# Optimization experiments

Hardware: AMD Instinct MI355X
Metric: run time of the kernel (lower is better)

## Reference

```python
import jax, jax.numpy as jnp
import numpy as np

B, S_F, S_H, S_W = 1, 4, 32, 32
S = S_F * S_H * S_W            # 4096 video tokens
DIM, HEADS = 1536, 12
HD = DIM // HEADS              # 128
EPS = 1e-6


def _rope_angles(max_pos, dim_half):
    inv = 1.0 / (10000.0 ** (np.arange(dim_half, dtype=np.float32) / dim_half))
    return (np.arange(max_pos, dtype=np.float32)[:, None] * inv[None, :]).astype(np.float32)


def setup_inputs():
    key = jax.random.key(0)
    ks = jax.random.split(key, 6)
    w = lambda k: jax.random.normal(k, (DIM, DIM), jnp.float32) * (DIM ** -0.5)
    c = HD // 2
    f0, f1 = c - 2 * (c // 3), c // 3   # 22, 21 (Wan rope split for F/H/W)
    freqs = jnp.asarray(np.concatenate(
        [_rope_angles(1024, f0), _rope_angles(1024, f1), _rope_angles(1024, f1)], axis=1))
    return dict(
        x=jax.random.normal(ks[0], (B, S, DIM), jnp.float32),
        seq_lens=jnp.full((B,), S, jnp.int32),
        grid_sizes=jnp.array([[S_F, S_H, S_W]], jnp.int32),
        freqs=freqs,
        t=500,
        Wq=w(ks[1]), bq=jnp.zeros((DIM,), jnp.float32),
        Wk=w(ks[2]), bk=jnp.zeros((DIM,), jnp.float32),
        Wv=w(ks[3]), bv=jnp.zeros((DIM,), jnp.float32),
        Wo=w(ks[4]), bo=jnp.zeros((DIM,), jnp.float32),
        gq=jnp.ones((DIM,), jnp.float32),
        gk=jnp.ones((DIM,), jnp.float32),
    )


def _rmsnorm(x, g):
    return x * jax.lax.rsqrt(jnp.mean(x * x, axis=-1, keepdims=True) + EPS) * g


def _rope_apply(x, cos, sin):
    # x: [B,S,n,d]; cos/sin: [S, d//2]; rotate interleaved (even, odd) pairs
    b, s, n, d = x.shape
    xr = x.reshape(b, s, n, d // 2, 2)
    xe, xo = xr[..., 0], xr[..., 1]
    c = cos[None, :, None, :]
    sn = sin[None, :, None, :]
    return jnp.stack([xe * c - xo * sn, xe * sn + xo * c], axis=-1).reshape(b, s, n, d)


def _rope_tables(grid_sizes, freqs):
    F, H, W = [int(v) for v in np.asarray(grid_sizes)[0]]
    c = HD // 2
    f0, f1 = c - 2 * (c // 3), c // 3
    ang = jnp.concatenate([
        jnp.broadcast_to(freqs[:F, :f0][:, None, None, :], (F, H, W, f0)),
        jnp.broadcast_to(freqs[:H, f0:f0 + f1][None, :, None, :], (F, H, W, f1)),
        jnp.broadcast_to(freqs[:W, f0 + f1:][None, None, :, :], (F, H, W, f1)),
    ], axis=-1).reshape(F * H * W, c)  # [S, d//2]
    return jnp.cos(ang), jnp.sin(ang)


def reference(x, seq_lens, grid_sizes, freqs, t, Wq, bq, Wk, bk, Wv, bv, Wo, bo, gq, gk):
    b, s = x.shape[:2]
    cos, sin = _rope_tables(grid_sizes, freqs)

    q = _rmsnorm(x @ Wq.T + bq, gq).reshape(b, s, HEADS, HD)
    k = _rmsnorm(x @ Wk.T + bk, gk).reshape(b, s, HEADS, HD)
    v = (x @ Wv.T + bv).reshape(b, s, HEADS, HD)
    q = _rope_apply(q, cos, sin)
    k = _rope_apply(k, cos, sin)

    scores = jnp.einsum('bqhd,bkhd->bhqk', q, k) * (HD ** -0.5)  # [B,H,S,S]
    kmask = jnp.arange(s)[None, :] < seq_lens[:, None]           # varlen key mask
    scores = jnp.where(kmask[:, None, None, :], scores, -jnp.inf)
    attn = jax.nn.softmax(scores, axis=-1)
    out = jnp.einsum('bhqk,bkhd->bqhd', attn, v).reshape(b, s, DIM)
    return out @ Wo.T + bo
```

## Files before the change

### kernel.cpp

```cpp
#include <hip/hip_runtime.h>
#include <hip/hip_bf16.h>

#define S 4096
#define DIM 1536
#define HEADS 12
#define HD 128
#define CHALF 64
#define NQKV 4608

typedef unsigned short u16;
typedef unsigned int u32;
typedef __attribute__((ext_vector_type(8))) short bf16x8;
typedef __attribute__((ext_vector_type(4))) float f32x4;
typedef __attribute__((ext_vector_type(16))) float f32x16;

__device__ __forceinline__ u16 f2b(float f) {
    u32 u = __float_as_uint(f);
    u32 r = (u + 0x7fffu + ((u >> 16) & 1u)) >> 16;
    return (u16)r;
}
__device__ __forceinline__ float b2f(u16 b) {
    return __uint_as_float(((u32)b) << 16);
}
__device__ __forceinline__ u32 pack2(float a, float b) {
    u32 lo = (__float_as_uint(a) + 0x8000u) >> 16;
    u32 hi = (__float_as_uint(b) + 0x8000u) & 0xffff0000u;
    return lo | hi;
}
__device__ __forceinline__ void gld_lds16(const u16* g, u16* l) {
    __builtin_amdgcn_global_load_lds((const __attribute__((address_space(1))) void*)g,
                                     (__attribute__((address_space(3))) void*)l, 16, 0, 0);
}

__global__ void k_cvt_all(const float4* __restrict__ x, const float4* __restrict__ wq,
                          const float4* __restrict__ wk, const float4* __restrict__ wv,
                          const float4* __restrict__ wo,
                          ushort4* __restrict__ xb, ushort4* __restrict__ wqkv,
                          ushort4* __restrict__ wob) {
    const int N4X = S * DIM / 4, N4W = DIM * DIM / 4;
    int i = blockIdx.x * 256 + threadIdx.x;
    const float4* src; ushort4* dst; int off;
    if (i < N4X) { src = x; dst = xb; off = i; }
    else {
        int j = i - N4X;
        int w = j / N4W; off = j - w * N4W;
        if (w == 0)      { src = wq; dst = wqkv; }
        else if (w == 1) { src = wk; dst = wqkv + N4W; }
        else if (w == 2) { src = wv; dst = wqkv + 2 * N4W; }
        else             { src = wo; dst = wob; }
    }
    float4 v = src[off];
    ushort4 o;
    o.x = f2b(v.x); o.y = f2b(v.y); o.z = f2b(v.z); o.w = f2b(v.w);
    dst[off] = o;
}

__global__ void k_tables(const float* __restrict__ freqs, const int* __restrict__ grid_sizes,
                         float* __restrict__ cosT, float* __restrict__ sinT) {
    int idx = blockIdx.x * 256 + threadIdx.x;
    if (idx >= S * CHALF) return;
    int s = idx >> 6;
    int i = idx & 63;
    int H = grid_sizes[1], W = grid_sizes[2];
    int hw = H * W;
    int f = s / hw;
    int rem = s - f * hw;
    int h = rem / W;
    int w = rem - h * W;
    const int f0 = 22, f1 = 21;
    int pos = (i < f0) ? f : ((i < f0 + f1) ? h : w);
    float ang = freqs[pos * CHALF + i];
    cosT[idx] = cosf(ang);
    sinT[idx] = sinf(ang);
}

template<int OUT_BF16, int QKV>
__global__ __launch_bounds__(256, 2) void k_gemm(const u16* __restrict__ A, const u16* __restrict__ W,
                                                 const float* __restrict__ b0, const float* __restrict__ b1,
                                                 const float* __restrict__ b2,
                                                 void* __restrict__ Cout, int N, int K, int ldc) {
    __shared__ u16 As[128 * 32];
    __shared__ u16 Bs[128 * 32];
    int tid = threadIdx.x;
    int lane = tid & 63, wave = tid >> 6;
    int wm = wave >> 1, wn = wave & 1;
    int quad = lane >> 4, l16 = lane & 15;
    int rowBase = blockIdx.y * 128;
    int colBase = blockIdx.x * 128;
    int lr = lane >> 2, lc = (lane & 3) << 3;

    f32x4 acc[4][4] = {};

    for (int kb = 0; kb < K; kb += 32) {
        __syncthreads();
#pragma unroll
        for (int c = 0; c < 2; c++) {
            int rrel = wave * 32 + c * 16;
            gld_lds16(A + (size_t)(rowBase + rrel + lr) * K + kb + lc, As + rrel * 32);
            gld_lds16(W + (size_t)(colBase + rrel + lr) * K + kb + lc, Bs + rrel * 32);
        }
        __syncthreads();

        bf16x8 a[4], b[4];
#pragma unroll
        for (int mi = 0; mi < 4; mi++)
            a[mi] = *(const bf16x8*)(As + (wm * 64 + mi * 16 + l16) * 32 + quad * 8);
#pragma unroll
        for (int ni = 0; ni < 4; ni++)
            b[ni] = *(const bf16x8*)(Bs + (wn * 64 + ni * 16 + l16) * 32 + quad * 8);
#pragma unroll
        for (int mi = 0; mi < 4; mi++)
#pragma unroll
            for (int ni = 0; ni < 4; ni++)
                acc[mi][ni] = __builtin_amdgcn_mfma_f32_16x16x32_bf16(a[mi], b[ni], acc[mi][ni], 0, 0, 0);
    }

#pragma unroll
    for (int mi = 0; mi < 4; mi++) {
#pragma unroll
        for (int ni = 0; ni < 4; ni++) {
            int col = colBase + wn * 64 + ni * 16 + l16;
            float bv;
            if (QKV) {
                int third = colBase / DIM;
                const float* bp = (third == 0) ? b0 : ((third == 1) ? b1 : b2);
                bv = bp[col - third * DIM];
            } else {
                bv = b0[col];
            }
#pragma unroll
            for (int r = 0; r < 4; r++) {
                int row = rowBase + wm * 64 + mi * 16 + quad * 4 + r;
                float v = acc[mi][ni][r] + bv;
                if (OUT_BF16)
                    ((u16*)Cout)[(size_t)row * ldc + col] = f2b(v);
                else
                    ((float*)Cout)[(size_t)row * ldc + col] = v;
            }
        }
    }
}

__global__ __launch_bounds__(256) void k_normrope(u16* __restrict__ qkvp, const float* __restrict__ gq,
                                                  const float* __restrict__ gk,
                                                  const float* __restrict__ cosT, const float* __restrict__ sinT,
                                                  float qscale) {
    int s = blockIdx.x;
    int which = blockIdx.y;
    const float* g = which ? gk : gq;
    float scale = which ? 1.0f : qscale;
    int tid = threadIdx.x;
    int lane = tid & 63, wave = tid >> 6;
    u32* row = (u32*)(qkvp + (size_t)s * NQKV + which * DIM);

    int w0 = tid, w1 = tid + 256, w2 = tid + 512;
    u32 p0 = row[w0], p1 = row[w1], p2 = row[w2];
    float e0 = b2f(p0 & 0xffff), o0 = b2f(p0 >> 16);
    float e1 = b2f(p1 & 0xffff), o1 = b2f(p1 >> 16);
    float e2 = b2f(p2 & 0xffff), o2 = b2f(p2 >> 16);
    float ss = e0 * e0 + o0 * o0 + e1 * e1 + o1 * o1 + e2 * e2 + o2 * o2;

    __shared__ float wsum[4];
    for (int off = 32; off; off >>= 1) ss += __shfl_down(ss, off);
    if (lane == 0) wsum[wave] = ss;
    __syncthreads();
    float tot = wsum[0] + wsum[1] + wsum[2] + wsum[3];
    float r = rsqrtf(tot * (1.0f / DIM) + 1e-6f) * scale;

    const float* cr = cosT + (size_t)s * CHALF;
    const float* sr = sinT + (size_t)s * CHALF;
#pragma unroll
    for (int j = 0; j < 3; j++) {
        int p = (j == 0) ? w0 : (j == 1) ? w1 : w2;
        float e = (j == 0) ? e0 : (j == 1) ? e1 : e2;
        float o = (j == 0) ? o0 : (j == 1) ? o1 : o2;
        int i = p & 63;
        float c = cr[i], sn = sr[i];
        e = e * r * g[2 * p];
        o = o * r * g[2 * p + 1];
        float ne = e * c - o * sn;
        float no = e * sn + o * c;
        row[p] = (u32)f2b(ne) | ((u32)f2b(no) << 16);
    }
}

__global__ void k_transpose(const u16* __restrict__ src, u16* __restrict__ dst) {
    __shared__ u16 t[32][33];
    int bx = blockIdx.x;
    int by = blockIdx.y;
    int tx = threadIdx.x, ty = threadIdx.y;
#pragma unroll
    for (int i = 0; i < 4; i++)
        t[ty + i * 8][tx] = src[(size_t)(by * 32 + ty + i * 8) * NQKV + bx * 32 + tx];
    __syncthreads();
#pragma unroll
    for (int i = 0; i < 4; i++)
        dst[(size_t)(bx * 32 + ty + i * 8) * S + by * 32 + tx] = t[tx][ty + i * 8];
}

#define FM 16.5f
__global__ __launch_bounds__(256, 3) void k_attn(const u16* __restrict__ qkv, const u16* __restrict__ vt,
                                                 u16* __restrict__ O0, u16* __restrict__ O1,
                                                 float* __restrict__ lT,
                                                 const int* __restrict__ seq_lens) {
    int h = blockIdx.y;
    int q0 = blockIdx.x * 128;
    int p = blockIdx.z;
    int kh0 = p * (S / 2);
    int tid = threadIdx.x;
    int lane = tid & 63, wave = tid >> 6;
    int l31 = lane & 31, hi = lane >> 5;
    int seqlen = seq_lens[0];
    u16* Op = p ? O1 : O0;

    __shared__ u16 Ks[64 * 136];
    __shared__ u16 Vs[128 * 88];

    int qrow = q0 + wave * 32 + l31;
    bf16x8 qf[8];
#pragma unroll
    for (int c = 0; c < 8; c++)
        qf[c] = *(const bf16x8*)(qkv + (size_t)qrow * NQKV + h * HD + c * 16 + hi * 8);

    f32x16 o_acc[4] = {};
    float lsum = 0.f;

    for (int kt = 0; kt < S / 2; kt += 64) {
        int kbase = kh0 + kt;
        __syncthreads();
        {
            int r = tid >> 2, cc = (tid & 3) * 32;
            const u16* gk_ = qkv + (size_t)(kbase + r) * NQKV + DIM + h * HD + cc;
            u16* dk = Ks + r * 136 + cc;
#pragma unroll
            for (int u = 0; u < 4; u++)
                *(uint4*)(dk + u * 8) = *(const uint4*)(gk_ + u * 8);
            int dr = tid >> 3, dc = (tid & 7) * 8;
#pragma unroll
            for (int it = 0; it < 4; it++)
                *(uint4*)(Vs + (dr + it * 32) * 88 + dc) =
                    *(const uint4*)(vt + (size_t)(h * HD + dr + it * 32) * S + kbase + dc);
        }
        __syncthreads();

        f32x16 sc0 = {}, sc1 = {};
#pragma unroll
        for (int c = 0; c < 8; c++) {
            bf16x8 kf0 = *(const bf16x8*)(Ks + l31 * 136 + c * 16 + hi * 8);
            bf16x8 kf1 = *(const bf16x8*)(Ks + (32 + l31) * 136 + c * 16 + hi * 8);
            sc0 = __builtin_amdgcn_mfma_f32_32x32x16_bf16(kf0, qf[c], sc0, 0, 0, 0);
            sc1 = __builtin_amdgcn_mfma_f32_32x32x16_bf16(kf1, qf[c], sc1, 0, 0, 0);
        }

        bool tail = (kbase + 64 > seqlen);
        bf16x8 pfrag[4];
#pragma unroll
        for (int b = 0; b < 2; b++) {
            f32x16 s16 = b ? sc1 : sc0;
            u32 pk[4][2];
            if (!tail) {
#pragma unroll
                for (int g = 0; g < 4; g++) {
                    float e0 = __builtin_amdgcn_exp2f(s16[4 * g + 0] - FM);
                    float e1 = __builtin_amdgcn_exp2f(s16[4 * g + 1] - FM);
                    float e2 = __builtin_amdgcn_exp2f(s16[4 * g + 2] - FM);
                    float e3 = __builtin_amdgcn_exp2f(s16[4 * g + 3] - FM);
                    lsum += (e0 + e1) + (e2 + e3);
                    pk[g][0] = pack2(e0, e1);
                    pk[g][1] = pack2(e2, e3);
                }
            } else {
#pragma unroll
                for (int g = 0; g < 4; g++) {
                    float e[4];
#pragma unroll
                    for (int r = 0; r < 4; r++) {
                        int key = kbase + b * 32 + r + 8 * g + 4 * hi;
                        float v = __builtin_amdgcn_exp2f(s16[4 * g + r] - FM);
                        e[r] = (key < seqlen) ? v : 0.f;
                        lsum += e[r];
                    }
                    pk[g][0] = pack2(e[0], e[1]);
                    pk[g][1] = pack2(e[2], e[3]);
                }
            }
#pragma unroll
            for (int cc = 0; cc < 2; cc++) {
                int g0 = 2 * cc, g1 = 2 * cc + 1;
                u32 own0 = hi ? pk[g1][0] : pk[g0][0];
                u32 own1 = hi ? pk[g1][1] : pk[g0][1];
                u32 snd0 = hi ? pk[g0][0] : pk[g1][0];
                u32 snd1 = hi ? pk[g0][1] : pk[g1][1];
                u32 rcv0 = (u32)__shfl_xor((int)snd0, 32);
                u32 rcv1 = (u32)__shfl_xor((int)snd1, 32);
                union { u32 u[4]; bf16x8 v; } cvt2;
                cvt2.u[0] = hi ? rcv0 : own0;
                cvt2.u[1] = hi ? rcv1 : own1;
                cvt2.u[2] = hi ? own0 : rcv0;
                cvt2.u[3] = hi ? own1 : rcv1;
                pfrag[b * 2 + cc] = cvt2.v;
            }
        }

#pragma unroll
        for (int db = 0; db < 4; db++) {
#pragma unroll
            for (int c4 = 0; c4 < 4; c4++) {
                bf16x8 vf = *(const bf16x8*)(Vs + (db * 32 + l31) * 88 + c4 * 16 + hi * 8);
                o_acc[db] = __builtin_amdgcn_mfma_f32_32x32x16_bf16(vf, pfrag[c4], o_acc[db], 0, 0, 0);
            }
        }
    }

    float l_all = lsum + __shfl_xor(lsum, 32);
    float linv = 1.0f / l_all;
#pragma unroll
    for (int db = 0; db < 4; db++) {
#pragma unroll
        for (int g = 0; g < 4; g++) {
            int d0 = db * 32 + 8 * g + 4 * hi;
            u16 o4[4];
#pragma unroll
            for (int r = 0; r < 4; r++)
                o4[r] = f2b(o_acc[db][4 * g + r] * linv);
            *(uint2*)(Op + (size_t)qrow * DIM + h * HD + d0) = *(const uint2*)o4;
        }
    }
    if (!hi) lT[((size_t)p * HEADS + h) * S + qrow] = l_all;
}

__global__ __launch_bounds__(384) void k_combine(u16* __restrict__ O0, const u16* __restrict__ O1,
                                                 const float* __restrict__ lT) {
    int q = blockIdx.x;
    int tid = threadIdx.x;
    int h = tid >> 5;
    size_t base = (size_t)q * DIM + tid * 4;
    float l0 = lT[(size_t)h * S + q];
    float l1 = lT[(size_t)(HEADS + h) * S + q];
    float inv = 1.0f / (l0 + l1);
    float c0 = l0 * inv, c1 = l1 * inv;
    uint2 u0 = *(const uint2*)(O0 + base);
    uint2 u1 = *(const uint2*)(O1 + base);
    const u16* a = (const u16*)&u0;
    const u16* b = (const u16*)&u1;
    u16 o[4];
#pragma unroll
    for (int i = 0; i < 4; i++)
        o[i] = f2b(c0 * b2f(a[i]) + c1 * b2f(b[i]));
    *(uint2*)(O0 + base) = *(uint2*)o;
}

extern "C" void kernel_launch(void* const* d_in, const int* in_sizes, int n_in,
                              void* d_out, int out_size, void* d_ws, size_t ws_size,
                              hipStream_t stream) {
    const float* x = (const float*)d_in[0];
    const int* seq_lens = (const int*)d_in[1];
    const int* grid_sizes = (const int*)d_in[2];
    const float* freqs = (const float*)d_in[3];
    const float* Wq = (const float*)d_in[5];
    const float* bq = (const float*)d_in[6];
    const float* Wk = (const float*)d_in[7];
    const float* bk = (const float*)d_in[8];
    const float* Wv = (const float*)d_in[9];
    const float* bv = (const float*)d_in[10];
    const float* Wo = (const float*)d_in[11];
    const float* bo = (const float*)d_in[12];
    const float* gq = (const float*)d_in[13];
    const float* gk = (const float*)d_in[14];
    float* out = (float*)d_out;

    char* w = (char*)d_ws;
    u16* xb    = (u16*)w; w += (size_t)S * DIM * 2;
    u16* qkv   = (u16*)w; w += (size_t)S * NQKV * 2;
    u16* Wqkvb = (u16*)w; w += (size_t)3 * DIM * DIM * 2;
    u16* Wob   = (u16*)w; w += (size_t)DIM * DIM * 2;
    u16* ab    = (u16*)w; w += (size_t)S * DIM * 2;
    u16* O1    = (u16*)w; w += (size_t)S * DIM * 2;
    float* cosT = (float*)w; w += (size_t)S * CHALF * 4;
    float* sinT = (float*)w; w += (size_t)S * CHALF * 4;
    float* lT  = (float*)w; w += (size_t)2 * HEADS * S * 4;
    u16* vt = Wqkvb;

    const float qscale = 0.08838834764831845f * 1.44269504088896341f;

    const int N4X = S * DIM / 4, N4W = DIM * DIM / 4;
    k_cvt_all<<<(N4X + 4 * N4W) / 256, 256, 0, stream>>>(
        (const float4*)x, (const float4*)Wq, (const float4*)Wk, (const float4*)Wv, (const float4*)Wo,
        (ushort4*)xb, (ushort4*)Wqkvb, (ushort4*)Wob);
    k_tables<<<(S * CHALF + 255) / 256, 256, 0, stream>>>(freqs, grid_sizes, cosT, sinT);

    k_gemm<1, 1><<<dim3(NQKV / 128, S / 128), 256, 0, stream>>>(
        xb, Wqkvb, bq, bk, bv, qkv, NQKV, DIM, NQKV);

    k_normrope<<<dim3(S, 2), 256, 0, stream>>>(qkv, gq, gk, cosT, sinT, qscale);

    k_transpose<<<dim3(DIM / 32, S / 32), dim3(32, 8), 0, stream>>>(qkv + 2 * DIM, vt);

    k_attn<<<dim3(S / 128, HEADS, 2), 256, 0, stream>>>(qkv, vt, ab, O1, lT, seq_lens);

    k_combine<<<S, 384, 0, stream>>>(ab, O1, lT);

    k_gemm<0, 0><<<dim3(DIM / 128, S / 128), 256, 0, stream>>>(
        ab, Wob, bo, bo, bo, out, DIM, DIM, DIM);
}
```

Before: 429.9 us.

## Split attention keys four ways, swizzle LDS with direct loads, narrow output GEMM tile

The attention kernel now splits the key range into four parts instead of two, which doubles the block count and raises the occupancy hint to 4. The partial outputs are written into buffers that are no longer needed (xb and the V slot of qkv), and the combine step is extended to merge all four. K and V tiles are now loaded straight into LDS with an XOR swizzle instead of padded rows. The output projection uses a 128x64 tile so more blocks are launched. The costs are extra combine traffic and more partial-result writes.

```diff
diff --git a/kernel.cpp b/kernel.cpp
--- a/kernel.cpp
+++ b/kernel.cpp
@@ -74,52 +74,65 @@
     sinT[idx] = sinf(ang);
 }
 
-template<int OUT_BF16, int QKV>
+template<int TN, int OUT_BF16, int QKV>
 __global__ __launch_bounds__(256, 2) void k_gemm(const u16* __restrict__ A, const u16* __restrict__ W,
                                                  const float* __restrict__ b0, const float* __restrict__ b1,
                                                  const float* __restrict__ b2,
                                                  void* __restrict__ Cout, int N, int K, int ldc) {
     __shared__ u16 As[128 * 32];
-    __shared__ u16 Bs[128 * 32];
+    __shared__ u16 Bs[TN * 32];
     int tid = threadIdx.x;
     int lane = tid & 63, wave = tid >> 6;
-    int wm = wave >> 1, wn = wave & 1;
     int quad = lane >> 4, l16 = lane & 15;
     int rowBase = blockIdx.y * 128;
-    int colBase = blockIdx.x * 128;
+    int colBase = blockIdx.x * TN;
     int lr = lane >> 2, lc = (lane & 3) << 3;
 
-    f32x4 acc[4][4] = {};
+    constexpr int MI = (TN == 128) ? 4 : 2;
+    int wm = (TN == 128) ? (wave >> 1) : wave;
+    int wn = (TN == 128) ? (wave & 1) : 0;
+
+    f32x4 acc[MI][4] = {};
 
     for (int kb = 0; kb < K; kb += 32) {
         __syncthreads();
-#pragma unroll
-        for (int c = 0; c < 2; c++) {
-            int rrel = wave * 32 + c * 16;
-            gld_lds16(A + (size_t)(rowBase + rrel + lr) * K + kb + lc, As + rrel * 32);
-            gld_lds16(W + (size_t)(colBase + rrel + lr) * K + kb + lc, Bs + rrel * 32);
+        if (TN == 128) {
+#pragma unroll
+            for (int c = 0; c < 2; c++) {
+                int rrel = wave * 32 + c * 16;
+                gld_lds16(A + (size_t)(rowBase + rrel + lr) * K + kb + lc, As + rrel * 32);
+                gld_lds16(W + (size_t)(colBase + rrel + lr) * K + kb + lc, Bs + rrel * 32);
+            }
+        } else {
+            gld_lds16(A + (size_t)(rowBase + wave * 32 + lr) * K + kb + lc, As + (wave * 32) * 32);
+            gld_lds16(A + (size_t)(rowBase + wave * 32 + 16 + lr) * K + kb + lc, As + (wave * 32 + 16) * 32);
+            gld_lds16(W + (size_t)(colBase + wave * 16 + lr) * K + kb + lc, Bs + (wave * 16) * 32);
         }
         __syncthreads();
 
-        bf16x8 a[4], b[4];
-#pragma unroll
-        for (int mi = 0; mi < 4; mi++)
-            a[mi] = *(const bf16x8*)(As + (wm * 64 + mi * 16 + l16) * 32 + quad * 8);
-#pragma unroll
-        for (int ni = 0; ni < 4; ni++)
-            b[ni] = *(const bf16x8*)(Bs + (wn * 64 + ni * 16 + l16) * 32 + quad * 8);
-#pragma unroll
-        for (int mi = 0; mi < 4; mi++)
+        bf16x8 a[MI], b[4];
+#pragma unroll
+        for (int mi = 0; mi < MI; mi++) {
+            int row = (TN == 128) ? (wm * 64 + mi * 16 + l16) : (wave * 32 + mi * 16 + l16);
+            a[mi] = *(const bf16x8*)(As + row * 32 + quad * 8);
+        }
+#pragma unroll
+        for (int ni = 0; ni < 4; ni++) {
+            int row = (TN == 128) ? (wn * 64 + ni * 16 + l16) : (ni * 16 + l16);
+            b[ni] = *(const bf16x8*)(Bs + row * 32 + quad * 8);
+        }
+#pragma unroll
+        for (int mi = 0; mi < MI; mi++)
 #pragma unroll
             for (int ni = 0; ni < 4; ni++)
                 acc[mi][ni] = __builtin_amdgcn_mfma_f32_16x16x32_bf16(a[mi], b[ni], acc[mi][ni], 0, 0, 0);
     }
 
 #pragma unroll
-    for (int mi = 0; mi < 4; mi++) {
+    for (int mi = 0; mi < MI; mi++) {
 #pragma unroll
         for (int ni = 0; ni < 4; ni++) {
-            int col = colBase + wn * 64 + ni * 16 + l16;
+            int col = colBase + ((TN == 128) ? wn * 64 : 0) + ni * 16 + l16;
             float bv;
             if (QKV) {
                 int third = colBase / DIM;
@@ -130,7 +143,7 @@
             }
 #pragma unroll
             for (int r = 0; r < 4; r++) {
-                int row = rowBase + wm * 64 + mi * 16 + quad * 4 + r;
+                int row = rowBase + ((TN == 128) ? wm * 64 : wave * 32) + mi * 16 + quad * 4 + r;
                 float v = acc[mi][ni][r] + bv;
                 if (OUT_BF16)
                     ((u16*)Cout)[(size_t)row * ldc + col] = f2b(v);
@@ -199,22 +212,32 @@
 }
 
 #define FM 16.5f
-__global__ __launch_bounds__(256, 3) void k_attn(const u16* __restrict__ qkv, const u16* __restrict__ vt,
+__global__ __launch_bounds__(256, 4) void k_attn(const u16* __restrict__ qkv, const u16* __restrict__ vt,
                                                  u16* __restrict__ O0, u16* __restrict__ O1,
+                                                 u16* __restrict__ O2, u16* __restrict__ O3,
                                                  float* __restrict__ lT,
                                                  const int* __restrict__ seq_lens) {
     int h = blockIdx.y;
     int q0 = blockIdx.x * 128;
     int p = blockIdx.z;
-    int kh0 = p * (S / 2);
+    int kh0 = p * (S / 4);
     int tid = threadIdx.x;
     int lane = tid & 63, wave = tid >> 6;
     int l31 = lane & 31, hi = lane >> 5;
+    int l31x = l31 & 7;
     int seqlen = seq_lens[0];
-    u16* Op = p ? O1 : O0;
-
-    __shared__ u16 Ks[64 * 136];
-    __shared__ u16 Vs[128 * 88];
+
+    __shared__ u16 Ks[64 * 128];
+    __shared__ u16 Vs[128 * 64];
+
+    size_t koff_[4], voff_[4];
+#pragma unroll
+    for (int it = 0; it < 4; it++) {
+        int kr = wave * 16 + it * 4 + (lane >> 4);
+        koff_[it] = (size_t)kr * NQKV + DIM + h * HD + (((lane & 15) ^ (kr & 7)) << 3);
+        int vr = wave * 32 + it * 8 + (lane >> 3);
+        voff_[it] = (size_t)(h * HD + vr) * S + (((lane & 7) ^ (vr & 7)) << 3);
+    }
 
     int qrow = q0 + wave * 32 + l31;
     bf16x8 qf[8];
@@ -225,29 +248,26 @@
     f32x16 o_acc[4] = {};
     float lsum = 0.f;
 
-    for (int kt = 0; kt < S / 2; kt += 64) {
+    for (int kt = 0; kt < S / 4; kt += 64) {
         int kbase = kh0 + kt;
         __syncthreads();
         {
-            int r = tid >> 2, cc = (tid & 3) * 32;
-            const u16* gk_ = qkv + (size_t)(kbase + r) * NQKV + DIM + h * HD + cc;
-            u16* dk = Ks + r * 136 + cc;
-#pragma unroll
-            for (int u = 0; u < 4; u++)
-                *(uint4*)(dk + u * 8) = *(const uint4*)(gk_ + u * 8);
-            int dr = tid >> 3, dc = (tid & 7) * 8;
+            size_t kb = (size_t)kbase * NQKV;
 #pragma unroll
             for (int it = 0; it < 4; it++)
-                *(uint4*)(Vs + (dr + it * 32) * 88 + dc) =
-                    *(const uint4*)(vt + (size_t)(h * HD + dr + it * 32) * S + kbase + dc);
+                gld_lds16(qkv + kb + koff_[it], Ks + (wave * 16 + it * 4) * 128);
+#pragma unroll
+            for (int it = 0; it < 4; it++)
+                gld_lds16(vt + kbase + voff_[it], Vs + (wave * 32 + it * 8) * 64);
         }
         __syncthreads();
 
         f32x16 sc0 = {}, sc1 = {};
 #pragma unroll
         for (int c = 0; c < 8; c++) {
-            bf16x8 kf0 = *(const bf16x8*)(Ks + l31 * 136 + c * 16 + hi * 8);
-            bf16x8 kf1 = *(const bf16x8*)(Ks + (32 + l31) * 136 + c * 16 + hi * 8);
+            int j = 2 * c + hi;
+            bf16x8 kf0 = *(const bf16x8*)(Ks + l31 * 128 + ((j ^ l31x) << 3));
+            bf16x8 kf1 = *(const bf16x8*)(Ks + (32 + l31) * 128 + ((j ^ l31x) << 3));
             sc0 = __builtin_amdgcn_mfma_f32_32x32x16_bf16(kf0, qf[c], sc0, 0, 0, 0);
             sc1 = __builtin_amdgcn_mfma_f32_32x32x16_bf16(kf1, qf[c], sc1, 0, 0, 0);
         }
@@ -306,11 +326,15 @@
         for (int db = 0; db < 4; db++) {
 #pragma unroll
             for (int c4 = 0; c4 < 4; c4++) {
-                bf16x8 vf = *(const bf16x8*)(Vs + (db * 32 + l31) * 88 + c4 * 16 + hi * 8);
+                int j = 2 * c4 + hi;
+                bf16x8 vf = *(const bf16x8*)(Vs + (db * 32 + l31) * 64 + ((j ^ l31x) << 3));
                 o_acc[db] = __builtin_amdgcn_mfma_f32_32x32x16_bf16(vf, pfrag[c4], o_acc[db], 0, 0, 0);
             }
         }
     }
+
+    u16* Op = (p == 0) ? O0 : (p == 1) ? O1 : (p == 2) ? O2 : O3;
+    size_t ldO = (p == 3) ? NQKV : DIM;
 
     float l_all = lsum + __shfl_xor(lsum, 32);
     float linv = 1.0f / l_all;
@@ -323,31 +347,39 @@
 #pragma unroll
             for (int r = 0; r < 4; r++)
                 o4[r] = f2b(o_acc[db][4 * g + r] * linv);
-            *(uint2*)(Op + (size_t)qrow * DIM + h * HD + d0) = *(const uint2*)o4;
+            *(uint2*)(Op + (size_t)qrow * ldO + h * HD + d0) = *(const uint2*)o4;
         }
     }
     if (!hi) lT[((size_t)p * HEADS + h) * S + qrow] = l_all;
 }
 
 __global__ __launch_bounds__(384) void k_combine(u16* __restrict__ O0, const u16* __restrict__ O1,
+                                                 const u16* __restrict__ O2, const u16* __restrict__ O3,
                                                  const float* __restrict__ lT) {
     int q = blockIdx.x;
     int tid = threadIdx.x;
     int h = tid >> 5;
-    size_t base = (size_t)q * DIM + tid * 4;
-    float l0 = lT[(size_t)h * S + q];
-    float l1 = lT[(size_t)(HEADS + h) * S + q];
-    float inv = 1.0f / (l0 + l1);
-    float c0 = l0 * inv, c1 = l1 * inv;
-    uint2 u0 = *(const uint2*)(O0 + base);
-    uint2 u1 = *(const uint2*)(O1 + base);
+    float l0 = lT[(size_t)(0 * HEADS + h) * S + q];
+    float l1 = lT[(size_t)(1 * HEADS + h) * S + q];
+    float l2 = lT[(size_t)(2 * HEADS + h) * S + q];
+    float l3 = lT[(size_t)(3 * HEADS + h) * S + q];
+    float inv = 1.0f / (l0 + l1 + l2 + l3);
+    float c0 = l0 * inv, c1 = l1 * inv, c2 = l2 * inv, c3 = l3 * inv;
+    size_t b0 = (size_t)q * DIM + tid * 4;
+    size_t b3 = (size_t)q * NQKV + tid * 4;
+    uint2 u0 = *(const uint2*)(O0 + b0);
+    uint2 u1 = *(const uint2*)(O1 + b0);
+    uint2 u2 = *(const uint2*)(O2 + b0);
+    uint2 u3 = *(const uint2*)(O3 + b3);
     const u16* a = (const u16*)&u0;
     const u16* b = (const u16*)&u1;
+    const u16* c = (const u16*)&u2;
+    const u16* d = (const u16*)&u3;
     u16 o[4];
 #pragma unroll
     for (int i = 0; i < 4; i++)
-        o[i] = f2b(c0 * b2f(a[i]) + c1 * b2f(b[i]));
-    *(uint2*)(O0 + base) = *(uint2*)o;
+        o[i] = f2b(c0 * b2f(a[i]) + c1 * b2f(b[i]) + c2 * b2f(c[i]) + c3 * b2f(d[i]));
+    *(uint2*)(O0 + b0) = *(uint2*)o;
 }
 
 extern "C" void kernel_launch(void* const* d_in, const int* in_sizes, int n_in,
@@ -378,8 +410,10 @@
     u16* O1    = (u16*)w; w += (size_t)S * DIM * 2;
     float* cosT = (float*)w; w += (size_t)S * CHALF * 4;
     float* sinT = (float*)w; w += (size_t)S * CHALF * 4;
-    float* lT  = (float*)w; w += (size_t)2 * HEADS * S * 4;
+    float* lT  = (float*)w; w += (size_t)4 * HEADS * S * 4;
     u16* vt = Wqkvb;
+    u16* O2 = xb;
+    u16* O3 = qkv + 2 * DIM;
 
     const float qscale = 0.08838834764831845f * 1.44269504088896341f;
 
@@ -389,17 +423,17 @@
         (ushort4*)xb, (ushort4*)Wqkvb, (ushort4*)Wob);
     k_tables<<<(S * CHALF + 255) / 256, 256, 0, stream>>>(freqs, grid_sizes, cosT, sinT);
 
-    k_gemm<1, 1><<<dim3(NQKV / 128, S / 128), 256, 0, stream>>>(
+    k_gemm<128, 1, 1><<<dim3(NQKV / 128, S / 128), 256, 0, stream>>>(
         xb, Wqkvb, bq, bk, bv, qkv, NQKV, DIM, NQKV);
 
     k_normrope<<<dim3(S, 2), 256, 0, stream>>>(qkv, gq, gk, cosT, sinT, qscale);
 
     k_transpose<<<dim3(DIM / 32, S / 32), dim3(32, 8), 0, stream>>>(qkv + 2 * DIM, vt);
 
-    k_attn<<<dim3(S / 128, HEADS, 2), 256, 0, stream>>>(qkv, vt, ab, O1, lT, seq_lens);
-
-    k_combine<<<S, 384, 0, stream>>>(ab, O1, lT);
-
-    k_gemm<0, 0><<<dim3(DIM / 128, S / 128), 256, 0, stream>>>(
+    k_attn<<<dim3(S / 128, HEADS, 4), 256, 0, stream>>>(qkv, vt, ab, O1, O2, O3, lT, seq_lens);
+
+    k_combine<<<S, 384, 0, stream>>>(ab, O1, O2, O3, lT);
+
+    k_gemm<64, 0, 0><<<dim3(DIM / 64, S / 128), 256, 0, stream>>>(
         ab, Wob, bo, bo, bo, out, DIM, DIM, DIM);
 }
```

New measurement: 713.9 us. 66.1% more time.

## Prefetch next K/V tile into registers in attention; narrow output GEMM tiles

Applied to the files above, without the earlier changes.

The attention kernel now loads the next K and V tile from global memory into registers while the current tile is being computed, and stores those registers to shared memory at the start of the next iteration. This hides global load latency behind MFMA work. Its occupancy hint rises from 3 to 4 blocks per CU. The output projection GEMM moves to a 128x64 tile variant, which doubles its grid to 384 blocks for better CU fill, at the cost of less reuse per block. The extra prefetch registers may cause spills or stop the higher occupancy target from being reached.

```diff
diff --git a/kernel.cpp b/kernel.cpp
--- a/kernel.cpp
+++ b/kernel.cpp
@@ -74,52 +74,65 @@
     sinT[idx] = sinf(ang);
 }
 
-template<int OUT_BF16, int QKV>
+template<int TN, int OUT_BF16, int QKV>
 __global__ __launch_bounds__(256, 2) void k_gemm(const u16* __restrict__ A, const u16* __restrict__ W,
                                                  const float* __restrict__ b0, const float* __restrict__ b1,
                                                  const float* __restrict__ b2,
                                                  void* __restrict__ Cout, int N, int K, int ldc) {
     __shared__ u16 As[128 * 32];
-    __shared__ u16 Bs[128 * 32];
+    __shared__ u16 Bs[TN * 32];
     int tid = threadIdx.x;
     int lane = tid & 63, wave = tid >> 6;
-    int wm = wave >> 1, wn = wave & 1;
     int quad = lane >> 4, l16 = lane & 15;
     int rowBase = blockIdx.y * 128;
-    int colBase = blockIdx.x * 128;
+    int colBase = blockIdx.x * TN;
     int lr = lane >> 2, lc = (lane & 3) << 3;
 
-    f32x4 acc[4][4] = {};
+    constexpr int MI = (TN == 128) ? 4 : 2;
+    int wm = (TN == 128) ? (wave >> 1) : wave;
+    int wn = (TN == 128) ? (wave & 1) : 0;
+
+    f32x4 acc[MI][4] = {};
 
     for (int kb = 0; kb < K; kb += 32) {
         __syncthreads();
-#pragma unroll
-        for (int c = 0; c < 2; c++) {
-            int rrel = wave * 32 + c * 16;
-            gld_lds16(A + (size_t)(rowBase + rrel + lr) * K + kb + lc, As + rrel * 32);
-            gld_lds16(W + (size_t)(colBase + rrel + lr) * K + kb + lc, Bs + rrel * 32);
+        if (TN == 128) {
+#pragma unroll
+            for (int c = 0; c < 2; c++) {
+                int rrel = wave * 32 + c * 16;
+                gld_lds16(A + (size_t)(rowBase + rrel + lr) * K + kb + lc, As + rrel * 32);
+                gld_lds16(W + (size_t)(colBase + rrel + lr) * K + kb + lc, Bs + rrel * 32);
+            }
+        } else {
+            gld_lds16(A + (size_t)(rowBase + wave * 32 + lr) * K + kb + lc, As + (wave * 32) * 32);
+            gld_lds16(A + (size_t)(rowBase + wave * 32 + 16 + lr) * K + kb + lc, As + (wave * 32 + 16) * 32);
+            gld_lds16(W + (size_t)(colBase + wave * 16 + lr) * K + kb + lc, Bs + (wave * 16) * 32);
         }
         __syncthreads();
 
-        bf16x8 a[4], b[4];
-#pragma unroll
-        for (int mi = 0; mi < 4; mi++)
-            a[mi] = *(const bf16x8*)(As + (wm * 64 + mi * 16 + l16) * 32 + quad * 8);
-#pragma unroll
-        for (int ni = 0; ni < 4; ni++)
-            b[ni] = *(const bf16x8*)(Bs + (wn * 64 + ni * 16 + l16) * 32 + quad * 8);
-#pragma unroll
-        for (int mi = 0; mi < 4; mi++)
+        bf16x8 a[MI], b[4];
+#pragma unroll
+        for (int mi = 0; mi < MI; mi++) {
+            int row = (TN == 128) ? (wm * 64 + mi * 16 + l16) : (wave * 32 + mi * 16 + l16);
+            a[mi] = *(const bf16x8*)(As + row * 32 + quad * 8);
+        }
+#pragma unroll
+        for (int ni = 0; ni < 4; ni++) {
+            int row = (TN == 128) ? (wn * 64 + ni * 16 + l16) : (ni * 16 + l16);
+            b[ni] = *(const bf16x8*)(Bs + row * 32 + quad * 8);
+        }
+#pragma unroll
+        for (int mi = 0; mi < MI; mi++)
 #pragma unroll
             for (int ni = 0; ni < 4; ni++)
                 acc[mi][ni] = __builtin_amdgcn_mfma_f32_16x16x32_bf16(a[mi], b[ni], acc[mi][ni], 0, 0, 0);
     }
 
 #pragma unroll
-    for (int mi = 0; mi < 4; mi++) {
+    for (int mi = 0; mi < MI; mi++) {
 #pragma unroll
         for (int ni = 0; ni < 4; ni++) {
-            int col = colBase + wn * 64 + ni * 16 + l16;
+            int col = colBase + ((TN == 128) ? wn * 64 : 0) + ni * 16 + l16;
             float bv;
             if (QKV) {
                 int third = colBase / DIM;
@@ -130,7 +143,7 @@
             }
 #pragma unroll
             for (int r = 0; r < 4; r++) {
-                int row = rowBase + wm * 64 + mi * 16 + quad * 4 + r;
+                int row = rowBase + ((TN == 128) ? wm * 64 : wave * 32) + mi * 16 + quad * 4 + r;
                 float v = acc[mi][ni][r] + bv;
                 if (OUT_BF16)
                     ((u16*)Cout)[(size_t)row * ldc + col] = f2b(v);
@@ -199,7 +212,7 @@
 }
 
 #define FM 16.5f
-__global__ __launch_bounds__(256, 3) void k_attn(const u16* __restrict__ qkv, const u16* __restrict__ vt,
+__global__ __launch_bounds__(256, 4) void k_attn(const u16* __restrict__ qkv, const u16* __restrict__ vt,
                                                  u16* __restrict__ O0, u16* __restrict__ O1,
                                                  float* __restrict__ lT,
                                                  const int* __restrict__ seq_lens) {
@@ -216,6 +229,11 @@
     __shared__ u16 Ks[64 * 136];
     __shared__ u16 Vs[128 * 88];
 
+    int skr = tid >> 2, skc = (tid & 3) * 32;
+    int svr = tid >> 3, svc = (tid & 7) * 8;
+    const u16* kgbase = qkv + DIM + h * HD + (size_t)skr * NQKV + skc;
+    const u16* vgbase = vt + (size_t)(h * HD + svr) * S + svc;
+
     int qrow = q0 + wave * 32 + l31;
     bf16x8 qf[8];
 #pragma unroll
@@ -224,24 +242,38 @@
 
     f32x16 o_acc[4] = {};
     float lsum = 0.f;
+
+    uint4 kreg[4], vreg[4];
+#pragma unroll
+    for (int u = 0; u < 4; u++)
+        kreg[u] = *(const uint4*)(kgbase + (size_t)kh0 * NQKV + u * 8);
+#pragma unroll
+    for (int it = 0; it < 4; it++)
+        vreg[it] = *(const uint4*)(vgbase + (size_t)(it * 32) * S + kh0);
 
     for (int kt = 0; kt < S / 2; kt += 64) {
         int kbase = kh0 + kt;
         __syncthreads();
         {
-            int r = tid >> 2, cc = (tid & 3) * 32;
-            const u16* gk_ = qkv + (size_t)(kbase + r) * NQKV + DIM + h * HD + cc;
-            u16* dk = Ks + r * 136 + cc;
+            u16* dk = Ks + skr * 136 + skc;
 #pragma unroll
             for (int u = 0; u < 4; u++)
-                *(uint4*)(dk + u * 8) = *(const uint4*)(gk_ + u * 8);
-            int dr = tid >> 3, dc = (tid & 7) * 8;
+                *(uint4*)(dk + u * 8) = kreg[u];
 #pragma unroll
             for (int it = 0; it < 4; it++)
-                *(uint4*)(Vs + (dr + it * 32) * 88 + dc) =
-                    *(const uint4*)(vt + (size_t)(h * HD + dr + it * 32) * S + kbase + dc);
+                *(uint4*)(Vs + (svr + it * 32) * 88 + svc) = vreg[it];
         }
         __syncthreads();
+
+        if (kt + 64 < S / 2) {
+            int nb = kbase + 64;
+#pragma unroll
+            for (int u = 0; u < 4; u++)
+                kreg[u] = *(const uint4*)(kgbase + (size_t)nb * NQKV + u * 8);
+#pragma unroll
+            for (int it = 0; it < 4; it++)
+                vreg[it] = *(const uint4*)(vgbase + (size_t)(it * 32) * S + nb);
+        }
 
         f32x16 sc0 = {}, sc1 = {};
 #pragma unroll
@@ -389,7 +421,7 @@
         (ushort4*)xb, (ushort4*)Wqkvb, (ushort4*)Wob);
     k_tables<<<(S * CHALF + 255) / 256, 256, 0, stream>>>(freqs, grid_sizes, cosT, sinT);
 
-    k_gemm<1, 1><<<dim3(NQKV / 128, S / 128), 256, 0, stream>>>(
+    k_gemm<128, 1, 1><<<dim3(NQKV / 128, S / 128), 256, 0, stream>>>(
         xb, Wqkvb, bq, bk, bv, qkv, NQKV, DIM, NQKV);
 
     k_normrope<<<dim3(S, 2), 256, 0, stream>>>(qkv, gq, gk, cosT, sinT, qscale);
@@ -400,6 +432,6 @@
 
     k_combine<<<S, 384, 0, stream>>>(ab, O1, lT);
 
-    k_gemm<0, 0><<<dim3(DIM / 128, S / 128), 256, 0, stream>>>(
+    k_gemm<64, 0, 0><<<dim3(DIM / 64, S / 128), 256, 0, stream>>>(
         ab, Wob, bo, bo, bo, out, DIM, DIM, DIM);
 }
```

After: 747.3 us. 1.74x slower.
